# Kernel optimization log

Hardware: AMD Instinct MI355X
Metric: run time of the kernel (lower is better)

Reference implementation:

```python
import jax, jax.numpy as jnp
import numpy as np

B, S, I, H = 64, 1024, 256, 256

def setup_inputs() -> dict:
    key = jax.random.key(0)
    k1, k2, k3 = jax.random.split(key, 3)
    x = jax.random.normal(k1, (B, S, I), dtype=jnp.float32)
    W = jax.random.normal(k2, (4 * H, H + I), dtype=jnp.float32) * (1.0 / np.sqrt(H + I))
    b = jax.random.normal(k3, (4 * H,), dtype=jnp.float32) * 0.01
    return {"x": x, "W": W, "b": b}

def reference(x, W, b):
    batch, seq_len, input_size = x.shape
    hidden = W.shape[1] - input_size
    # torch concat order is (hidden, x): first H columns of W act on h, rest on x
    W_h = W[:, :hidden]          # [4H, H]
    W_x = W[:, hidden:]          # [4H, I]
    # precompute input projections for all timesteps: [B, S, 4H]
    x_proj = jnp.einsum('bsi,gi->bsg', x, W_x) + b

    h0 = jnp.zeros((batch, hidden), dtype=x.dtype)
    c0 = jnp.zeros((batch, hidden), dtype=x.dtype)

    def step(carry, xp_t):
        h, c = carry
        gates = h @ W_h.T + xp_t                     # [B, 4H]
        f, i, g, o = jnp.split(gates, 4, axis=1)     # chunk order: forget, input, convert, output
        f = jax.nn.sigmoid(f)
        i = jax.nn.sigmoid(i)
        g = jnp.tanh(g)
        o = jax.nn.sigmoid(o)
        c_new = f * c + i * g
        h_new = o * jnp.tanh(c_new)
        return (h_new, c_new), h_new

    (h_fin, c_fin), outs = jax.lax.scan(step, (h0, c0), jnp.swapaxes(x_proj, 0, 1))
    outputs = jnp.swapaxes(outs, 0, 1)               # [B, S, H]
    return outputs, (h_fin, c_fin)
```

## Files before the change

kernel.cpp:

```cpp
#include <hip/hip_runtime.h>

typedef __attribute__((ext_vector_type(8))) short short8;
typedef __attribute__((ext_vector_type(4))) float f32x4;
typedef __attribute__((ext_vector_type(4))) unsigned u32x4;

__device__ __forceinline__ unsigned short f2bf(float f) {
  unsigned int u = __float_as_uint(f);
  u = (u + 0x7fffu + ((u >> 16) & 1u)) >> 16;
  return (unsigned short)u;
}

__device__ __forceinline__ void xp_store(float* p, float v) { *p = v; }
__device__ __forceinline__ void xp_store(unsigned short* p, float v) { *p = f2bf(v); }
__device__ __forceinline__ float xp_load(const float* p) { return *p; }
__device__ __forceinline__ float xp_load(const unsigned short* p) {
  return __uint_as_float(((unsigned int)*p) << 16);
}

__global__ void prep_wx(const float* __restrict__ W, unsigned int* __restrict__ Wx2) {
  int i = blockIdx.x * 256 + threadIdx.x;
  int g = i >> 7, kk = i & 127;
  float lo = W[(size_t)g * 512 + 256 + 2 * kk];
  float hi = W[(size_t)g * 512 + 256 + 2 * kk + 1];
  Wx2[i] = (unsigned int)f2bf(lo) | ((unsigned int)f2bf(hi) << 16);
}

__global__ void prep_wh(const float* __restrict__ W, unsigned int* __restrict__ Wh2) {
  int i = blockIdx.x * 256 + threadIdx.x;
  int r = i >> 7, kk = i & 127;
  float lo = W[(size_t)r * 512 + 2 * kk];
  float hi = W[(size_t)r * 512 + 2 * kk + 1];
  Wh2[i] = (unsigned int)f2bf(lo) | ((unsigned int)f2bf(hi) << 16);
}

template <typename XPT>
__global__ __launch_bounds__(256, 4) void gemm_xp(const float* __restrict__ x,
                                                  const unsigned int* __restrict__ Wx2,
                                                  const float* __restrict__ bias,
                                                  XPT* __restrict__ xp) {
  __shared__ unsigned short As[128][40];
  __shared__ unsigned short Bs[128][40];
  const int m0 = blockIdx.y * 128, n0 = blockIdx.x * 128;
  const int tid = threadIdx.x, lane = tid & 63, w = tid >> 6;
  const int wr = w >> 1, wc = w & 1;
  const int r16 = lane & 15, kq = lane >> 4;
  f32x4 acc[4][4];
#pragma unroll
  for (int m = 0; m < 4; m++)
#pragma unroll
    for (int n = 0; n < 4; n++)
#pragma unroll
      for (int j = 0; j < 4; j++) acc[m][n][j] = 0.f;

  for (int kb = 0; kb < 256; kb += 32) {
    __syncthreads();
#pragma unroll
    for (int i = 0; i < 4; i++) {
      int idx = tid + i * 256;
      int row = idx >> 3, c4 = idx & 7;
      float4 v = *(const float4*)(x + (size_t)(m0 + row) * 256 + kb + c4 * 4);
      ushort4 s;
      s.x = f2bf(v.x); s.y = f2bf(v.y); s.z = f2bf(v.z); s.w = f2bf(v.w);
      *(ushort4*)&As[row][c4 * 4] = s;
    }
#pragma unroll
    for (int i = 0; i < 2; i++) {
      int idx = tid + i * 256;
      int row = idx >> 2, c = idx & 3;
      uint4 v = *(const uint4*)(Wx2 + (size_t)(n0 + row) * 128 + (kb >> 1) + c * 4);
      *(uint4*)&Bs[row][c * 8] = v;
    }
    __syncthreads();
    short8 a[4], bb[4];
#pragma unroll
    for (int m = 0; m < 4; m++)
      a[m] = *(const short8*)&As[wr * 64 + m * 16 + r16][kq * 8];
#pragma unroll
    for (int n = 0; n < 4; n++)
      bb[n] = *(const short8*)&Bs[wc * 64 + n * 16 + r16][kq * 8];
#pragma unroll
    for (int m = 0; m < 4; m++)
#pragma unroll
      for (int n = 0; n < 4; n++)
        acc[m][n] = __builtin_amdgcn_mfma_f32_16x16x32_bf16(a[m], bb[n], acc[m][n], 0, 0, 0);
  }
#pragma unroll
  for (int n = 0; n < 4; n++) {
    int gn = n0 + wc * 64 + n * 16 + r16;
    float bi = bias[gn];
#pragma unroll
    for (int m = 0; m < 4; m++) {
      int gm = m0 + wr * 64 + m * 16 + kq * 4;
#pragma unroll
      for (int j = 0; j < 4; j++) {
        xp_store(&xp[(size_t)(gm + j) * 1024 + gn], acc[m][n][j] + bi);
      }
    }
  }
}

template <typename XPT>
__global__ __launch_bounds__(1024, 4) void lstm_rec(const unsigned* __restrict__ Wh2,
                                                    const XPT* __restrict__ xp,
                                                    float* __restrict__ out) {
  __shared__ unsigned wo[1024 * 36];
  __shared__ unsigned hb2[2][128];

  const int tid = threadIdx.x;
  const int b = blockIdx.x;
  const int u = tid >> 2, p = tid & 3;

  const unsigned* wf_p = Wh2 + (size_t)(0 * 256 + u) * 128 + (p << 5);
  const unsigned* wi_p = Wh2 + (size_t)(1 * 256 + u) * 128 + (p << 5);
  const unsigned* wg_p = Wh2 + (size_t)(2 * 256 + u) * 128 + (p << 5);
  const unsigned* wo_p = Wh2 + (size_t)(3 * 256 + u) * 128 + (p << 5);
  u32x4 wf0 = *(const u32x4*)(wf_p + 0),  wf1 = *(const u32x4*)(wf_p + 4);
  u32x4 wf2 = *(const u32x4*)(wf_p + 8),  wf3 = *(const u32x4*)(wf_p + 12);
  u32x4 wf4 = *(const u32x4*)(wf_p + 16), wf5 = *(const u32x4*)(wf_p + 20);
  u32x4 wf6 = *(const u32x4*)(wf_p + 24), wf7 = *(const u32x4*)(wf_p + 28);
  u32x4 wi0 = *(const u32x4*)(wi_p + 0),  wi1 = *(const u32x4*)(wi_p + 4);
  u32x4 wi2 = *(const u32x4*)(wi_p + 8),  wi3 = *(const u32x4*)(wi_p + 12);
  u32x4 wi4 = *(const u32x4*)(wi_p + 16), wi5 = *(const u32x4*)(wi_p + 20);
  u32x4 wi6 = *(const u32x4*)(wi_p + 24), wi7 = *(const u32x4*)(wi_p + 28);
  u32x4 wg0 = *(const u32x4*)(wg_p + 0),  wg1 = *(const u32x4*)(wg_p + 4);
  u32x4 wg2 = *(const u32x4*)(wg_p + 8),  wg3 = *(const u32x4*)(wg_p + 12);
  u32x4 wg4 = *(const u32x4*)(wg_p + 16), wg5 = *(const u32x4*)(wg_p + 20);
  u32x4 wg6 = *(const u32x4*)(wg_p + 24), wg7 = *(const u32x4*)(wg_p + 28);

#pragma unroll
  for (int j = 0; j < 8; j++) {
    u32x4 v = *(const u32x4*)(wo_p + (j << 2));
    *(u32x4*)&wo[tid * 36 + (j << 2)] = v;
  }
  if (tid < 256) ((unsigned*)hb2)[tid] = 0u;

  const size_t xpb = (size_t)b << 10;
  float xv0, xv1, xv2, xv3;
  {
    const XPT* xr = &xp[xpb * 1024 + u];
    xv0 = xp_load(xr); xv1 = xp_load(xr + 256);
    xv2 = xp_load(xr + 512); xv3 = xp_load(xr + 768);
  }
  float c = 0.f;
  __syncthreads();

  for (int t = 0; t < 1024; t++) {
    const unsigned* hrow = &hb2[(t + 1) & 1][p << 5];
    const unsigned* orow = &wo[tid * 36];

    float a0 = 0.f, a1 = 0.f, a2 = 0.f, a3 = 0.f;
#define DOT2(ACC, WD, HD) \
  asm("v_dot2_f32_bf16 %0, %1, %2, %0" : "+v"(ACC) : "v"(WD), "v"(HD))
#define STEPJ(J, WF, WI, WG)                                   \
  {                                                            \
    u32x4 hj = *(const u32x4*)(hrow + (J << 2));               \
    u32x4 oj = *(const u32x4*)(orow + (J << 2));               \
    DOT2(a0, WF[0], hj[0]); DOT2(a0, WF[1], hj[1]);            \
    DOT2(a0, WF[2], hj[2]); DOT2(a0, WF[3], hj[3]);            \
    DOT2(a1, WI[0], hj[0]); DOT2(a1, WI[1], hj[1]);            \
    DOT2(a1, WI[2], hj[2]); DOT2(a1, WI[3], hj[3]);            \
    DOT2(a2, WG[0], hj[0]); DOT2(a2, WG[1], hj[1]);            \
    DOT2(a2, WG[2], hj[2]); DOT2(a2, WG[3], hj[3]);            \
    DOT2(a3, oj[0], hj[0]); DOT2(a3, oj[1], hj[1]);            \
    DOT2(a3, oj[2], hj[2]); DOT2(a3, oj[3], hj[3]);            \
  }
    STEPJ(0, wf0, wi0, wg0) STEPJ(1, wf1, wi1, wg1)
    STEPJ(2, wf2, wi2, wg2) STEPJ(3, wf3, wi3, wg3)
    STEPJ(4, wf4, wi4, wg4) STEPJ(5, wf5, wi5, wg5)
    STEPJ(6, wf6, wi6, wg6) STEPJ(7, wf7, wi7, wg7)
#undef STEPJ
#undef DOT2

    a0 += __shfl_xor(a0, 1, 64); a0 += __shfl_xor(a0, 2, 64);
    a1 += __shfl_xor(a1, 1, 64); a1 += __shfl_xor(a1, 2, 64);
    a2 += __shfl_xor(a2, 1, 64); a2 += __shfl_xor(a2, 2, 64);
    a3 += __shfl_xor(a3, 1, 64); a3 += __shfl_xor(a3, 2, 64);

    float gf = a0 + xv0, gi = a1 + xv1, gg = a2 + xv2, go = a3 + xv3;
    float f = 1.f / (1.f + __expf(-gf));
    float ii = 1.f / (1.f + __expf(-gi));
    float eg = __expf(2.f * gg);
    float gt = (eg - 1.f) / (eg + 1.f);
    float o = 1.f / (1.f + __expf(-go));
    c = f * c + ii * gt;
    float ec = __expf(2.f * c);
    float tc = (ec - 1.f) / (ec + 1.f);
    float h = o * tc;

    float hu1 = __shfl(h, (tid & 63) + 4, 64);
    if (p == 0) {
      __builtin_nontemporal_store(h, &out[(xpb + t) * 256 + u]);
      if ((u & 1) == 0) {
        unsigned dw = (unsigned)f2bf(h) | ((unsigned)f2bf(hu1) << 16);
        hb2[t & 1][u >> 1] = dw;
      }
    }

    if (t < 1023) {
      const XPT* xr = &xp[(xpb + t + 1) * 1024 + u];
      xv0 = xp_load(xr); xv1 = xp_load(xr + 256);
      xv2 = xp_load(xr + 512); xv3 = xp_load(xr + 768);
    } else if (p == 0) {
      out[16777216 + b * 256 + u] = h;
      out[16777216 + 16384 + b * 256 + u] = c;
    }
    __syncthreads();
  }
}

extern "C" void kernel_launch(void* const* d_in, const int* in_sizes, int n_in,
                              void* d_out, int out_size, void* d_ws, size_t ws_size,
                              hipStream_t stream) {
  (void)in_sizes; (void)n_in; (void)out_size;
  const float* x = (const float*)d_in[0];
  const float* W = (const float*)d_in[1];
  const float* bias = (const float*)d_in[2];
  float* out = (float*)d_out;
  char* ws = (char*)d_ws;

  unsigned int* Wx2 = (unsigned int*)ws;
  unsigned int* Wh2 = (unsigned int*)(ws + 524288);
  char* xpmem = ws + 1048576;

  const size_t need32 = 1048576 + (size_t)65536 * 1024 * 4;

  prep_wx<<<512, 256, 0, stream>>>(W, Wx2);
  prep_wh<<<512, 256, 0, stream>>>(W, Wh2);

  if (ws_size >= need32) {
    gemm_xp<float><<<dim3(8, 512), 256, 0, stream>>>(x, Wx2, bias, (float*)xpmem);
    lstm_rec<float><<<64, 1024, 0, stream>>>(Wh2, (const float*)xpmem, out);
  } else {
    gemm_xp<unsigned short><<<dim3(8, 512), 256, 0, stream>>>(x, Wx2, bias,
                                                              (unsigned short*)xpmem);
    lstm_rec<unsigned short><<<64, 1024, 0, stream>>>(Wh2, (const unsigned short*)xpmem, out);
  }
}
```

Baseline: 2.519 ms.

## Relayout LDS weights and replicate hidden state per lane group to cut bank conflicts

The output-gate weights in LDS move from a padded row-per-thread layout to a column-major 64-bit layout indexed by thread id. Consecutive lanes now read consecutive 8-byte words, which is meant to remove LDS bank conflicts. The hidden-state buffer is replicated into four padded copies, one per p lane, so each quarter of lanes reads its own slice without colliding. All four lanes now write the packed h, and register weight loads are issued through inline asm so all of them are in flight before a single wait. The cost is more LDS writes per step and reliance on hand-written asm.

After: 2.747 ms. 9.1% more time.

```diff
diff --git a/kernel.cpp b/kernel.cpp
--- a/kernel.cpp
+++ b/kernel.cpp
@@ -103,8 +103,8 @@
 __global__ __launch_bounds__(1024, 4) void lstm_rec(const unsigned* __restrict__ Wh2,
                                                     const XPT* __restrict__ xp,
                                                     float* __restrict__ out) {
-  __shared__ unsigned wo[1024 * 36];
-  __shared__ unsigned hb2[2][128];
+  __shared__ unsigned long long wo64[16 * 1024];
+  __shared__ unsigned hb2[2][4][136];
 
   const int tid = threadIdx.x;
   const int b = blockIdx.x;
@@ -113,26 +113,34 @@
   const unsigned* wf_p = Wh2 + (size_t)(0 * 256 + u) * 128 + (p << 5);
   const unsigned* wi_p = Wh2 + (size_t)(1 * 256 + u) * 128 + (p << 5);
   const unsigned* wg_p = Wh2 + (size_t)(2 * 256 + u) * 128 + (p << 5);
+  u32x4 wf0, wf1, wf2, wf3, wf4, wf5, wf6, wf7;
+  u32x4 wi0, wi1, wi2, wi3, wi4, wi5, wi6, wi7;
+  u32x4 wg0, wg1, wg2, wg3, wg4, wg5, wg6, wg7;
+#define LOADROW(P, R0, R1, R2, R3, R4, R5, R6, R7)                    \
+  asm volatile("global_load_dwordx4 %0, %8, off\n\t"                  \
+               "global_load_dwordx4 %1, %8, off offset:16\n\t"        \
+               "global_load_dwordx4 %2, %8, off offset:32\n\t"        \
+               "global_load_dwordx4 %3, %8, off offset:48\n\t"        \
+               "global_load_dwordx4 %4, %8, off offset:64\n\t"        \
+               "global_load_dwordx4 %5, %8, off offset:80\n\t"        \
+               "global_load_dwordx4 %6, %8, off offset:96\n\t"        \
+               "global_load_dwordx4 %7, %8, off offset:112"           \
+               : "=&v"(R0), "=&v"(R1), "=&v"(R2), "=&v"(R3),          \
+                 "=&v"(R4), "=&v"(R5), "=&v"(R6), "=&v"(R7)           \
+               : "v"(P)                                               \
+               : "memory")
+  LOADROW(wf_p, wf0, wf1, wf2, wf3, wf4, wf5, wf6, wf7);
+  LOADROW(wi_p, wi0, wi1, wi2, wi3, wi4, wi5, wi6, wi7);
+  LOADROW(wg_p, wg0, wg1, wg2, wg3, wg4, wg5, wg6, wg7);
+#undef LOADROW
+  asm volatile("s_waitcnt vmcnt(0)" ::: "memory");
+
   const unsigned* wo_p = Wh2 + (size_t)(3 * 256 + u) * 128 + (p << 5);
-  u32x4 wf0 = *(const u32x4*)(wf_p + 0),  wf1 = *(const u32x4*)(wf_p + 4);
-  u32x4 wf2 = *(const u32x4*)(wf_p + 8),  wf3 = *(const u32x4*)(wf_p + 12);
-  u32x4 wf4 = *(const u32x4*)(wf_p + 16), wf5 = *(const u32x4*)(wf_p + 20);
-  u32x4 wf6 = *(const u32x4*)(wf_p + 24), wf7 = *(const u32x4*)(wf_p + 28);
-  u32x4 wi0 = *(const u32x4*)(wi_p + 0),  wi1 = *(const u32x4*)(wi_p + 4);
-  u32x4 wi2 = *(const u32x4*)(wi_p + 8),  wi3 = *(const u32x4*)(wi_p + 12);
-  u32x4 wi4 = *(const u32x4*)(wi_p + 16), wi5 = *(const u32x4*)(wi_p + 20);
-  u32x4 wi6 = *(const u32x4*)(wi_p + 24), wi7 = *(const u32x4*)(wi_p + 28);
-  u32x4 wg0 = *(const u32x4*)(wg_p + 0),  wg1 = *(const u32x4*)(wg_p + 4);
-  u32x4 wg2 = *(const u32x4*)(wg_p + 8),  wg3 = *(const u32x4*)(wg_p + 12);
-  u32x4 wg4 = *(const u32x4*)(wg_p + 16), wg5 = *(const u32x4*)(wg_p + 20);
-  u32x4 wg6 = *(const u32x4*)(wg_p + 24), wg7 = *(const u32x4*)(wg_p + 28);
-
-#pragma unroll
-  for (int j = 0; j < 8; j++) {
-    u32x4 v = *(const u32x4*)(wo_p + (j << 2));
-    *(u32x4*)&wo[tid * 36 + (j << 2)] = v;
-  }
-  if (tid < 256) ((unsigned*)hb2)[tid] = 0u;
+#pragma unroll
+  for (int j2 = 0; j2 < 16; j2++)
+    wo64[(j2 << 10) + tid] = *(const unsigned long long*)(wo_p + (j2 << 1));
+
+  for (int i = tid; i < 2 * 4 * 136; i += 1024) ((unsigned*)hb2)[i] = 0u;
 
   const size_t xpb = (size_t)b << 10;
   float xv0, xv1, xv2, xv3;
@@ -145,24 +153,24 @@
   __syncthreads();
 
   for (int t = 0; t < 1024; t++) {
-    const unsigned* hrow = &hb2[(t + 1) & 1][p << 5];
-    const unsigned* orow = &wo[tid * 36];
+    const unsigned* hrow = &hb2[(t + 1) & 1][p][p << 5];
 
     float a0 = 0.f, a1 = 0.f, a2 = 0.f, a3 = 0.f;
 #define DOT2(ACC, WD, HD) \
   asm("v_dot2_f32_bf16 %0, %1, %2, %0" : "+v"(ACC) : "v"(WD), "v"(HD))
-#define STEPJ(J, WF, WI, WG)                                   \
-  {                                                            \
-    u32x4 hj = *(const u32x4*)(hrow + (J << 2));               \
-    u32x4 oj = *(const u32x4*)(orow + (J << 2));               \
-    DOT2(a0, WF[0], hj[0]); DOT2(a0, WF[1], hj[1]);            \
-    DOT2(a0, WF[2], hj[2]); DOT2(a0, WF[3], hj[3]);            \
-    DOT2(a1, WI[0], hj[0]); DOT2(a1, WI[1], hj[1]);            \
-    DOT2(a1, WI[2], hj[2]); DOT2(a1, WI[3], hj[3]);            \
-    DOT2(a2, WG[0], hj[0]); DOT2(a2, WG[1], hj[1]);            \
-    DOT2(a2, WG[2], hj[2]); DOT2(a2, WG[3], hj[3]);            \
-    DOT2(a3, oj[0], hj[0]); DOT2(a3, oj[1], hj[1]);            \
-    DOT2(a3, oj[2], hj[2]); DOT2(a3, oj[3], hj[3]);            \
+#define STEPJ(J, WF, WI, WG)                                                \
+  {                                                                         \
+    u32x4 hj = *(const u32x4*)(hrow + ((J) << 2));                          \
+    unsigned long long o01 = wo64[((((J) << 1) + 0) << 10) + tid];          \
+    unsigned long long o23 = wo64[((((J) << 1) + 1) << 10) + tid];          \
+    DOT2(a0, WF[0], hj[0]); DOT2(a0, WF[1], hj[1]);                         \
+    DOT2(a0, WF[2], hj[2]); DOT2(a0, WF[3], hj[3]);                         \
+    DOT2(a1, WI[0], hj[0]); DOT2(a1, WI[1], hj[1]);                         \
+    DOT2(a1, WI[2], hj[2]); DOT2(a1, WI[3], hj[3]);                         \
+    DOT2(a2, WG[0], hj[0]); DOT2(a2, WG[1], hj[1]);                         \
+    DOT2(a2, WG[2], hj[2]); DOT2(a2, WG[3], hj[3]);                         \
+    DOT2(a3, (unsigned)o01, hj[0]); DOT2(a3, (unsigned)(o01 >> 32), hj[1]); \
+    DOT2(a3, (unsigned)o23, hj[2]); DOT2(a3, (unsigned)(o23 >> 32), hj[3]); \
   }
     STEPJ(0, wf0, wi0, wg0) STEPJ(1, wf1, wi1, wg1)
     STEPJ(2, wf2, wi2, wg2) STEPJ(3, wf3, wi3, wg3)
@@ -187,12 +195,16 @@
     float tc = (ec - 1.f) / (ec + 1.f);
     float h = o * tc;
 
-    float hu1 = __shfl(h, (tid & 63) + 4, 64);
+    float hu1 = __shfl(h, ((tid & 63) + 4) & 63, 64);
+    if ((u & 1) == 0) {
+      unsigned dw = (unsigned)f2bf(h) | ((unsigned)f2bf(hu1) << 16);
+      hb2[t & 1][p][u >> 1] = dw;
+    }
     if (p == 0) {
       __builtin_nontemporal_store(h, &out[(xpb + t) * 256 + u]);
-      if ((u & 1) == 0) {
-        unsigned dw = (unsigned)f2bf(h) | ((unsigned)f2bf(hu1) << 16);
-        hb2[t & 1][u >> 1] = dw;
+      if (t == 1023) {
+        out[16777216 + b * 256 + u] = h;
+        out[16777216 + 16384 + b * 256 + u] = c;
       }
     }
 
@@ -200,9 +212,6 @@
       const XPT* xr = &xp[(xpb + t + 1) * 1024 + u];
       xv0 = xp_load(xr); xv1 = xp_load(xr + 256);
       xv2 = xp_load(xr + 512); xv3 = xp_load(xr + 768);
-    } else if (p == 0) {
-      out[16777216 + b * 256 + u] = h;
-      out[16777216 + 16384 + b * 256 + u] = c;
     }
     __syncthreads();
   }
```
